# Optimization experiments

Measured on AMD Instinct MI355X. Metric: run time of the kernel, lower is better.

## Reference

```python
import jax, jax.numpy as jnp
import numpy as np

B, T, D = 32, 512, 512
MAX_LEN = 4096
DUR_MAX = 10


def setup_inputs() -> dict:
    key = jax.random.key(0)
    kx, kd = jax.random.split(key)
    x = jax.random.normal(kx, (B, T, D), dtype=jnp.float32)
    duration = jax.random.randint(kd, (B, T), 0, DUR_MAX, dtype=jnp.int64 if jax.config.read('jax_enable_x64') else jnp.int32)
    return {"x": x, "duration": duration, "max_len": MAX_LEN}


def reference(x, duration, max_len):
    # x: [B, T, D] phoneme-level features; duration: [B, T] frames per phoneme.
    # Equivalent of per-phoneme repeat_interleave + pad-to-max_len, done as a
    # single cumulative-duration index map + gather + mask (one fused pass).
    cum = jnp.cumsum(duration, axis=1)                      # [B, T] exclusive-of-0 cumsum
    frames = jnp.arange(max_len)                            # [M]
    # frame j belongs to phoneme i where cum[i-1] <= j < cum[i]
    idx = jax.vmap(lambda c: jnp.searchsorted(c, frames, side='right'))(cum)  # [B, M]
    idx = jnp.minimum(idx, x.shape[1] - 1)
    out = jnp.take_along_axis(x, idx[:, :, None], axis=1)   # [B, M, D]
    mel_len = cum[:, -1]                                    # [B] total expanded length
    mask = frames[None, :] < mel_len[:, None]               # [B, M] valid frames
    out = out * mask[:, :, None].astype(x.dtype)
    return out, mel_len
```

## Files before the change

### kernel.cpp

```cpp
#include <hip/hip_runtime.h>


typedef float f32x4 __attribute__((ext_vector_type(4)));
typedef int   i32x4 __attribute__((ext_vector_type(4)));

#define B_      32
#define T_      512
#define D_      512
#define MAXLEN_ 4096
#define TPB_    2
#define NBLK_   (B_ * T_ / TPB_)

__global__ void lr_fused_kernel(const float* __restrict__ x,
                                const int* __restrict__ dur,
                                float* __restrict__ out,
                                float* __restrict__ mel_out) {
    const int gid  = blockIdx.x;
    const int b    = gid >> 8;
    const int t0   = (gid & 255) * TPB_;
    const int sub  = threadIdx.x >> 7;
    const int half = (threadIdx.x >> 6) & 1;
    const int lane = threadIdx.x & 63;
    const int t    = t0 + sub;

    const i32x4* src = (const i32x4*)(dur + b * T_);
    i32x4 a = src[lane * 2];
    i32x4 c = src[lane * 2 + 1];
    int v0 = a.x,      v1 = v0 + a.y, v2 = v1 + a.z, v3 = v2 + a.w;
    int v4 = v3 + c.x, v5 = v4 + c.y, v6 = v5 + c.z, v7 = v6 + c.w;
    int s = v7;
    #pragma unroll
    for (int d = 1; d < 64; d <<= 1) {
        int u = __shfl_up(s, d, 64);
        if (lane >= d) s += u;
    }
    const int off = s - v7;
    v0 += off; v1 += off; v2 += off; v3 += off;
    v4 += off; v5 += off; v6 += off; v7 += off;

    const int mel = __shfl(v7, 63, 64);

    int e = t & 7;
    int sel = v0;
    sel = (e == 1) ? v1 : sel;  sel = (e == 2) ? v2 : sel;
    sel = (e == 3) ? v3 : sel;  sel = (e == 4) ? v4 : sel;
    sel = (e == 5) ? v5 : sel;  sel = (e == 6) ? v6 : sel;
    sel = (e == 7) ? v7 : sel;
    const int hi = __shfl(sel, t >> 3, 64);
    int lo = 0;
    if (t > 0) {
        int e2 = (t - 1) & 7;
        int sl = v0;
        sl = (e2 == 1) ? v1 : sl;  sl = (e2 == 2) ? v2 : sl;
        sl = (e2 == 3) ? v3 : sl;  sl = (e2 == 4) ? v4 : sl;
        sl = (e2 == 5) ? v5 : sl;  sl = (e2 == 6) ? v6 : sl;
        sl = (e2 == 7) ? v7 : sl;
        lo = __shfl(sl, (t - 1) >> 3, 64);
    }

    const int fl = half * 64 + lane;
    const int du = hi - lo;
    if (du > 0) {
        const f32x4 v = ((const f32x4*)(x + ((size_t)b * T_ + t) * D_))[fl];
        f32x4* dst = (f32x4*)(out + ((size_t)b * MAXLEN_ + lo) * D_) + fl;
        for (int i = 0; i < du; ++i)
            __builtin_nontemporal_store(v, dst + i * (D_ / 4));
    }

    const f32x4 z = {0.f, 0.f, 0.f, 0.f};
    for (int f = mel + t; f < MAXLEN_; f += T_) {
        f32x4* dz = (f32x4*)(out + ((size_t)b * MAXLEN_ + f) * D_) + fl;
        __builtin_nontemporal_store(z, dz);
    }

    if (t == 0 && threadIdx.x == 0) mel_out[b] = (float)mel;
}

extern "C" void kernel_launch(void* const* d_in, const int* in_sizes, int n_in,
                              void* d_out, int out_size, void* d_ws, size_t ws_size,
                              hipStream_t stream) {
    const float* x   = (const float*)d_in[0];
    const int*   dur = (const int*)d_in[1];

    float* out     = (float*)d_out;
    float* mel_out = out + (size_t)B_ * MAXLEN_ * D_;

    lr_fused_kernel<<<NBLK_, 256, 0, stream>>>(x, dur, out, mel_out);
}
```

Baseline: 54.48 us.

## Balance per-block frame work via shared frame-to-phoneme map over 8 phonemes

Each block now handles 8 phonemes instead of 2. It builds a shared-memory map from output frame to phoneme index, then has its two 128-thread halves stride over the block's output frames, so the store work per thread is even regardless of duration skew. Zero padding is split into contiguous chunks per block rather than strided rows. This trades a shared-memory map, a __syncthreads and a serial map fill by 8 threads for better load balance, and it launches 4x fewer blocks.

Result: slower. 59.64 us (+9.5%).

```diff
diff --git a/kernel.cpp b/kernel.cpp
--- a/kernel.cpp
+++ b/kernel.cpp
@@ -8,7 +8,8 @@
 #define T_      512
 #define D_      512
 #define MAXLEN_ 4096
-#define TPB_    2
+#define TPB_    8
+#define BPB_    (T_ / TPB_)
 #define NBLK_   (B_ * T_ / TPB_)
 
 __global__ void lr_fused_kernel(const float* __restrict__ x,
@@ -16,12 +17,14 @@
                                 float* __restrict__ out,
                                 float* __restrict__ mel_out) {
     const int gid  = blockIdx.x;
-    const int b    = gid >> 8;
-    const int t0   = (gid & 255) * TPB_;
+    const int b    = gid >> 6;
+    const int blk  = gid & (BPB_ - 1);
+    const int t0   = blk * TPB_;
     const int sub  = threadIdx.x >> 7;
-    const int half = (threadIdx.x >> 6) & 1;
+    const int fl   = threadIdx.x & 127;
     const int lane = threadIdx.x & 63;
-    const int t    = t0 + sub;
+
+    __shared__ int map[TPB_ * 9 + 8];
 
     const i32x4* src = (const i32x4*)(dur + b * T_);
     i32x4 a = src[lane * 2];
@@ -39,41 +42,48 @@
     v4 += off; v5 += off; v6 += off; v7 += off;
 
     const int mel = __shfl(v7, 63, 64);
+    const int L   = t0 >> 3;
+    int e0 = __shfl(v7, (L == 0) ? 0 : L - 1, 64);
+    if (t0 == 0) e0 = 0;
+    const int e1 = __shfl(v0, L, 64), e2 = __shfl(v1, L, 64);
+    const int e3 = __shfl(v2, L, 64), e4 = __shfl(v3, L, 64);
+    const int e5 = __shfl(v4, L, 64), e6 = __shfl(v5, L, 64);
+    const int e7 = __shfl(v6, L, 64), e8 = __shfl(v7, L, 64);
 
-    int e = t & 7;
-    int sel = v0;
-    sel = (e == 1) ? v1 : sel;  sel = (e == 2) ? v2 : sel;
-    sel = (e == 3) ? v3 : sel;  sel = (e == 4) ? v4 : sel;
-    sel = (e == 5) ? v5 : sel;  sel = (e == 6) ? v6 : sel;
-    sel = (e == 7) ? v7 : sel;
-    const int hi = __shfl(sel, t >> 3, 64);
-    int lo = 0;
-    if (t > 0) {
-        int e2 = (t - 1) & 7;
-        int sl = v0;
-        sl = (e2 == 1) ? v1 : sl;  sl = (e2 == 2) ? v2 : sl;
-        sl = (e2 == 3) ? v3 : sl;  sl = (e2 == 4) ? v4 : sl;
-        sl = (e2 == 5) ? v5 : sl;  sl = (e2 == 6) ? v6 : sl;
-        sl = (e2 == 7) ? v7 : sl;
-        lo = __shfl(sl, (t - 1) >> 3, 64);
+    if (threadIdx.x < TPB_) {
+        const int j = threadIdx.x;
+        int ej = e0, ej1 = e1;
+        ej  = (j == 1) ? e1 : ej;  ej1 = (j == 1) ? e2 : ej1;
+        ej  = (j == 2) ? e2 : ej;  ej1 = (j == 2) ? e3 : ej1;
+        ej  = (j == 3) ? e3 : ej;  ej1 = (j == 3) ? e4 : ej1;
+        ej  = (j == 4) ? e4 : ej;  ej1 = (j == 4) ? e5 : ej1;
+        ej  = (j == 5) ? e5 : ej;  ej1 = (j == 5) ? e6 : ej1;
+        ej  = (j == 6) ? e6 : ej;  ej1 = (j == 6) ? e7 : ej1;
+        ej  = (j == 7) ? e7 : ej;  ej1 = (j == 7) ? e8 : ej1;
+        for (int f = ej; f < ej1; ++f) map[f - e0] = j;
+    }
+    __syncthreads();
+
+    const int nf = min(e8, MAXLEN_) - e0;
+    const float* xblk = x + ((size_t)(b * T_ + t0)) * D_;
+    float*       oblk = out + ((size_t)b * MAXLEN_ + e0) * D_;
+    for (int fi = sub; fi < nf; fi += 2) {
+        const int j = map[fi];
+        const f32x4 v = ((const f32x4*)(xblk + (size_t)j * D_))[fl];
+        __builtin_nontemporal_store(v, (f32x4*)(oblk + (size_t)fi * D_) + fl);
     }
 
-    const int fl = half * 64 + lane;
-    const int du = hi - lo;
-    if (du > 0) {
-        const f32x4 v = ((const f32x4*)(x + ((size_t)b * T_ + t) * D_))[fl];
-        f32x4* dst = (f32x4*)(out + ((size_t)b * MAXLEN_ + lo) * D_) + fl;
-        for (int i = 0; i < du; ++i)
-            __builtin_nontemporal_store(v, dst + i * (D_ / 4));
+    const int nz    = (MAXLEN_ - mel > 0) ? (MAXLEN_ - mel) : 0;
+    const int chunk = (nz + BPB_ - 1) >> 6;
+    const int z0    = mel + blk * chunk;
+    const int z1    = min(z0 + chunk, MAXLEN_);
+    const f32x4 zv = {0.f, 0.f, 0.f, 0.f};
+    for (int f = z0 + sub; f < z1; f += 2) {
+        __builtin_nontemporal_store(
+            zv, (f32x4*)(out + ((size_t)b * MAXLEN_ + f) * D_) + fl);
     }
 
-    const f32x4 z = {0.f, 0.f, 0.f, 0.f};
-    for (int f = mel + t; f < MAXLEN_; f += T_) {
-        f32x4* dz = (f32x4*)(out + ((size_t)b * MAXLEN_ + f) * D_) + fl;
-        __builtin_nontemporal_store(z, dz);
-    }
-
-    if (t == 0 && threadIdx.x == 0) mel_out[b] = (float)mel;
+    if (blk == 0 && threadIdx.x == 0) mel_out[b] = (float)mel;
 }
 
 extern "C" void kernel_launch(void* const* d_in, const int* in_sizes, int n_in,
```

## Map one phoneme per wavefront with two vector loads per lane, prefetching x early

Applied to the files above, without the earlier changes.

Each 256-thread block now handles four phonemes, one per wavefront, and each lane writes two 16-byte chunks instead of one. The x row load is issued before the duration prefix scan so its latency overlaps the scan. The block count drops by half, which amortises the redundant per-block cumsum over more work. The row is now loaded even for zero-duration phonemes, and hi/lo are clamped to MAXLEN.

Result: no change. 55.40 us (+1.7%).

```diff
diff --git a/kernel.cpp b/kernel.cpp
--- a/kernel.cpp
+++ b/kernel.cpp
@@ -8,20 +8,23 @@
 #define T_      512
 #define D_      512
 #define MAXLEN_ 4096
-#define TPB_    2
-#define NBLK_   (B_ * T_ / TPB_)
+#define BPB_    128
+#define NBLK_   (B_ * BPB_)
 
 __global__ void lr_fused_kernel(const float* __restrict__ x,
                                 const int* __restrict__ dur,
                                 float* __restrict__ out,
                                 float* __restrict__ mel_out) {
     const int gid  = blockIdx.x;
-    const int b    = gid >> 8;
-    const int t0   = (gid & 255) * TPB_;
-    const int sub  = threadIdx.x >> 7;
-    const int half = (threadIdx.x >> 6) & 1;
+    const int b    = gid >> 7;
+    const int blk  = gid & (BPB_ - 1);
+    const int wid  = threadIdx.x >> 6;
     const int lane = threadIdx.x & 63;
-    const int t    = t0 + sub;
+    const int t    = blk * 4 + wid;
+
+    const f32x4* row = (const f32x4*)(x + ((size_t)b * T_ + t) * D_);
+    const f32x4 va = row[lane];
+    const f32x4 vb = row[lane + 64];
 
     const i32x4* src = (const i32x4*)(dur + b * T_);
     i32x4 a = src[lane * 2];
@@ -40,16 +43,16 @@
 
     const int mel = __shfl(v7, 63, 64);
 
-    int e = t & 7;
+    const int e = t & 7;
     int sel = v0;
     sel = (e == 1) ? v1 : sel;  sel = (e == 2) ? v2 : sel;
     sel = (e == 3) ? v3 : sel;  sel = (e == 4) ? v4 : sel;
     sel = (e == 5) ? v5 : sel;  sel = (e == 6) ? v6 : sel;
     sel = (e == 7) ? v7 : sel;
-    const int hi = __shfl(sel, t >> 3, 64);
+    int hi = __shfl(sel, t >> 3, 64);
     int lo = 0;
     if (t > 0) {
-        int e2 = (t - 1) & 7;
+        const int e2 = (t - 1) & 7;
         int sl = v0;
         sl = (e2 == 1) ? v1 : sl;  sl = (e2 == 2) ? v2 : sl;
         sl = (e2 == 3) ? v3 : sl;  sl = (e2 == 4) ? v4 : sl;
@@ -57,23 +60,23 @@
         sl = (e2 == 7) ? v7 : sl;
         lo = __shfl(sl, (t - 1) >> 3, 64);
     }
+    hi = min(hi, MAXLEN_);
+    lo = min(lo, MAXLEN_);
 
-    const int fl = half * 64 + lane;
-    const int du = hi - lo;
-    if (du > 0) {
-        const f32x4 v = ((const f32x4*)(x + ((size_t)b * T_ + t) * D_))[fl];
-        f32x4* dst = (f32x4*)(out + ((size_t)b * MAXLEN_ + lo) * D_) + fl;
-        for (int i = 0; i < du; ++i)
-            __builtin_nontemporal_store(v, dst + i * (D_ / 4));
+    f32x4* dst = (f32x4*)(out + ((size_t)b * MAXLEN_ + lo) * D_);
+    for (int i = 0; i < hi - lo; ++i) {
+        __builtin_nontemporal_store(va, dst + i * 128 + lane);
+        __builtin_nontemporal_store(vb, dst + i * 128 + lane + 64);
     }
 
     const f32x4 z = {0.f, 0.f, 0.f, 0.f};
     for (int f = mel + t; f < MAXLEN_; f += T_) {
-        f32x4* dz = (f32x4*)(out + ((size_t)b * MAXLEN_ + f) * D_) + fl;
-        __builtin_nontemporal_store(z, dz);
+        f32x4* dz = (f32x4*)(out + ((size_t)b * MAXLEN_ + f) * D_);
+        __builtin_nontemporal_store(z, dz + lane);
+        __builtin_nontemporal_store(z, dz + lane + 64);
     }
 
-    if (t == 0 && threadIdx.x == 0) mel_out[b] = (float)mel;
+    if (blk == 0 && threadIdx.x == 0) mel_out[b] = (float)mel;
 }
 
 extern "C" void kernel_launch(void* const* d_in, const int* in_sizes, int n_in,
```
